# Kernel optimization log

Measured on AMD Instinct MI355X. Metric: run time of the kernel, lower is better.

The kernel has to match this reference:

```python
import jax, jax.numpy as jnp
import numpy as np
from jax import lax

N_QUBITS = 4
N_QLAYERS = 2
C64 = jnp.complex64
PAIRS = [(i, j) for i in range(N_QUBITS) for j in range(i + 1, N_QUBITS)]  # 6 entangling pairs
CNOT = jnp.array([[1, 0, 0, 0], [0, 1, 0, 0], [0, 0, 0, 1], [0, 0, 1, 0]], dtype=C64)


def _rx(t):
    c = jnp.cos(t / 2).astype(C64)
    s = (-1j * jnp.sin(t / 2)).astype(C64)
    return jnp.stack([jnp.stack([c, s]), jnp.stack([s, c])])


def _ry(t):
    c = jnp.cos(t / 2).astype(C64)
    s = jnp.sin(t / 2).astype(C64)
    return jnp.stack([jnp.stack([c, -s]), jnp.stack([s, c])])


def _rz(t):
    e = jnp.exp(-1j * t.astype(C64) / 2)
    z = jnp.zeros_like(e)
    return jnp.stack([jnp.stack([e, z]), jnp.stack([z, jnp.conj(e)])])


def _apply_1q(state, M, w):
    # state: (B,2,2,2,2); M: (2,2) shared or (B,2,2) per-sample
    s = jnp.moveaxis(state, 1 + w, -1)
    if M.ndim == 2:
        s = jnp.einsum('b...j,ij->b...i', s, M)
    else:
        s = jnp.einsum('b...j,bij->b...i', s, M)
    return jnp.moveaxis(s, -1, 1 + w)


def _apply_2q(state, M4, c, t):
    # M4: (4,4) acting on (wire c, wire t)
    s = jnp.moveaxis(state, (1 + c, 1 + t), (-2, -1))
    sh = s.shape
    s = s.reshape(sh[:-2] + (4,))
    s = jnp.einsum('b...j,ij->b...i', s, M4)
    s = s.reshape(sh)
    return jnp.moveaxis(s, (-2, -1), (1 + c, 1 + t))


def _quantum_batched(angles, q_params):
    # angles: (B, 4) classical outputs; encoding is RY(angles*pi)
    B = angles.shape[0]
    state = jnp.zeros((B, 16), C64).at[:, 0].set(1.0).reshape(B, 2, 2, 2, 2)
    theta = angles * jnp.float32(np.pi)
    c = jnp.cos(theta / 2).astype(C64)  # (B,4)
    s = jnp.sin(theta / 2).astype(C64)
    for w in range(N_QUBITS):
        M = jnp.stack([jnp.stack([c[:, w], -s[:, w]], -1),
                       jnp.stack([s[:, w], c[:, w]], -1)], -2)  # (B,2,2)
        state = _apply_1q(state, M, w)
    per_layer = 3 * N_QUBITS + len(PAIRS)  # 18
    for l in range(N_QLAYERS):
        start = l * per_layer
        rot = q_params[start:start + 3 * N_QUBITS].reshape(N_QUBITS, 3)
        ent = q_params[start + 3 * N_QUBITS:start + per_layer]
        for q in range(N_QUBITS):
            M = _rz(rot[q, 2]) @ _ry(rot[q, 1]) @ _rx(rot[q, 0])
            state = _apply_1q(state, M, q)
        for k, (i, j) in enumerate(PAIRS):
            M4 = jnp.kron(jnp.eye(2, dtype=C64), _rz(ent[k])) @ CNOT  # CNOT then RZ on target
            state = _apply_2q(state, M4, i, j)
    probs = jnp.abs(state) ** 2  # (B,2,2,2,2)
    signs = jnp.array([1.0, -1.0], jnp.float32)
    zs = []
    for w in range(N_QUBITS):
        pw = jnp.moveaxis(probs, 1 + w, -1).reshape(B, -1, 2)
        zs.append((pw.sum(1) * signs).sum(-1))
    return jnp.stack(zs, -1)  # (B,4) PauliZ expvals


def _conv(x, w, b):
    y = lax.conv_general_dilated(x, w, (1, 1), ((1, 1), (1, 1)),
                                 dimension_numbers=('NCHW', 'OIHW', 'NCHW'))
    return y + b[None, :, None, None]


def _pool(x):
    return lax.reduce_window(x, -jnp.inf, lax.max, (1, 1, 2, 2), (1, 1, 2, 2), 'VALID')


def setup_inputs() -> dict:
    key = jax.random.key(0)
    ks = jax.random.split(key, 10)
    B = 4096
    return {
        'x': jax.random.normal(ks[0], (B, 1, 28, 28), jnp.float32),
        'conv1_w': jax.random.normal(ks[1], (16, 1, 3, 3), jnp.float32) * 0.1,
        'conv1_b': jax.random.normal(ks[2], (16,), jnp.float32) * 0.1,
        'conv2_w': jax.random.normal(ks[3], (32, 16, 3, 3), jnp.float32) * 0.05,
        'conv2_b': jax.random.normal(ks[4], (32,), jnp.float32) * 0.1,
        'dense_w': jax.random.normal(ks[5], (4, 1568), jnp.float32) * 0.02,
        'dense_b': jax.random.normal(ks[6], (4,), jnp.float32) * 0.1,
        'q_params': jax.random.normal(ks[7], (36,), jnp.float32) * 0.1,
        'post_w': jax.random.normal(ks[8], (10, 4), jnp.float32) * 0.5,
        'post_b': jax.random.normal(ks[9], (10,), jnp.float32) * 0.1,
    }


def reference(x, conv1_w, conv1_b, conv2_w, conv2_b, dense_w, dense_b, q_params, post_w, post_b):
    h = jax.nn.relu(_conv(x, conv1_w, conv1_b))
    h = _pool(h)
    h = jax.nn.relu(_conv(h, conv2_w, conv2_b))
    h = _pool(h)  # (B,32,7,7)
    h = h.reshape(h.shape[0], 32 * 7 * 7)
    # dropout is identity in eval mode
    angles = h @ dense_w.T + dense_b  # (B,4)
    z = _quantum_batched(angles, q_params)  # (B,4)
    return z @ post_w.T + post_b  # (B,10)
```

## Files before the change

kernel.cpp:

```cpp
#include <hip/hip_runtime.h>

#define PI_F 3.14159265358979323846f

typedef _Float16 half2v __attribute__((ext_vector_type(2)));
typedef _Float16 half4v __attribute__((ext_vector_type(4)));
typedef _Float16 half8v __attribute__((ext_vector_type(8)));
typedef float f32x4 __attribute__((ext_vector_type(4)));

struct C2 { float x, y; };
__device__ __forceinline__ C2 cmul(C2 a, C2 b) {
    return C2{a.x * b.x - a.y * b.y, a.x * b.y + a.y * b.x};
}

__device__ __forceinline__ void gate1(float& re, float& im, int l, int w,
                                      C2 m00, C2 m01, C2 m10, C2 m11) {
    int mask = 1 << (3 - w);
    float pre = __shfl_xor(re, mask, 64);
    float pim = __shfl_xor(im, mask, 64);
    bool b = (l & mask) != 0;
    C2 d = b ? m11 : m00;
    C2 o = b ? m10 : m01;
    float nre = d.x * re - d.y * im + o.x * pre - o.y * pim;
    float nim = d.x * im + d.y * re + o.x * pim + o.y * pre;
    re = nre; im = nim;
}

#define WS_C1B 2560
#define WS_DWT 2688
#define WS_GROT 8960
#define WS_GENT 9024

__global__ __launch_bounds__(256) void qnn_prep(
    const float* __restrict__ w1g, const float* __restrict__ w2g,
    const float* __restrict__ dwg, const float* __restrict__ qpg,
    float* __restrict__ ws)
{
    int t = threadIdx.x;
    for (int e = t; e < 640; e += 256) {
        int kstep = e >> 7, rem = e & 127;
        int ntile = rem >> 6, lane = rem & 63;
        int kq = lane >> 4, n = lane & 15;
        int oc = ntile * 16 + n;
        int pi = kstep * 2 + (kq >> 1);
        half8v h;
        #pragma unroll
        for (int jj = 0; jj < 8; ++jj) {
            int ic = (kq & 1) * 8 + jj;
            float v = (pi < 9) ? w2g[oc * 144 + ic * 9 + pi] : 0.f;
            h[jj] = (_Float16)v;
        }
        *(float4*)(ws + e * 4) = __builtin_bit_cast(float4, h);
    }
    if (t < 64) {
        int ky = t >> 4, n = t & 15;
        half4v h;
        #pragma unroll
        for (int j = 0; j < 4; ++j) {
            float v = (ky < 3 && j < 3) ? w1g[n * 9 + ky * 3 + j] : 0.f;
            h[j] = (_Float16)v;
        }
        *(float2*)(ws + WS_C1B + t * 2) = __builtin_bit_cast(float2, h);
    }
    for (int e = t; e < 1568; e += 256) {
        int quad = e >> 5, oc = e & 31;
        int src = oc * 49 + quad;
        float4 v = {dwg[src], dwg[1568 + src], dwg[3136 + src], dwg[4704 + src]};
        *(float4*)(ws + WS_DWT + e * 4) = v;
    }
    if (t < 8) {
        int layer = t >> 2, q = t & 3;
        int st = layer * 18;
        float a0 = qpg[st + 3 * q], a1 = qpg[st + 3 * q + 1], a2 = qpg[st + 3 * q + 2];
        float cx = cosf(0.5f * a0), sx = sinf(0.5f * a0);
        float cy = cosf(0.5f * a1), sy = sinf(0.5f * a1);
        float cz = cosf(0.5f * a2), sz = sinf(0.5f * a2);
        C2 T00{cy * cx,  sy * sx}, T01{-sy * cx, -cy * sx};
        C2 T10{sy * cx, -cy * sx}, T11{ cy * cx, -sy * sx};
        C2 E0{cz, -sz}, E1{cz, sz};
        C2 m00 = cmul(E0, T00), m01 = cmul(E0, T01);
        C2 m10 = cmul(E1, T10), m11 = cmul(E1, T11);
        float* gm = ws + WS_GROT + t * 8;
        gm[0] = m00.x; gm[1] = m00.y; gm[2] = m01.x; gm[3] = m01.y;
        gm[4] = m10.x; gm[5] = m10.y; gm[6] = m11.x; gm[7] = m11.y;
    }
    if (t >= 32 && t < 44) {
        int k = t - 32;
        float e = qpg[(k / 6) * 18 + 12 + (k % 6)];
        ws[WS_GENT + k * 2]     = cosf(0.5f * e);
        ws[WS_GENT + k * 2 + 1] = sinf(0.5f * e);
    }
}

__global__ __launch_bounds__(256, 4) void qnn_fused(
    const float* __restrict__ xg,
    const float* __restrict__ b1g, const float* __restrict__ b2g,
    const float* __restrict__ dbg,
    const float* __restrict__ wsc,
    const float* __restrict__ pwg, const float* __restrict__ pbg,
    float* __restrict__ out, int Btot)
{
    const int b4 = blockIdx.x << 2;
    const int t = threadIdx.x;
    const int lane = t & 63;
    const int wv = __builtin_amdgcn_readfirstlane(t >> 6);
    const int kq = lane >> 4;
    const int lm = lane & 15;

    __shared__ __align__(16) unsigned xhl[1200];
    __shared__ __align__(16) _Float16 p1f[16 * 20 * 24];
    __shared__ __align__(16) float angp[64];

    half8v bC2[5][2];
    {
        const float4* wsB = (const float4*)wsc;
        #pragma unroll
        for (int ks = 0; ks < 5; ++ks)
            #pragma unroll
            for (int nt = 0; nt < 2; ++nt)
                bC2[ks][nt] = __builtin_bit_cast(half8v, wsB[(ks * 2 + nt) * 64 + lane]);
    }
    half4v bC1 = __builtin_bit_cast(half4v, *(const float2*)(wsc + WS_C1B + lane * 2));
    float bias1 = b1g[lm];
    float b20 = b2g[lm], b21 = b2g[16 + lm];

    {
        uint4 z4 = {0u, 0u, 0u, 0u};
        uint4* p4 = (uint4*)p1f;
        #pragma unroll
        for (int j = 0; j < 4; ++j) {
            int i = t + j * 256;
            if (i < 960) p4[i] = z4;
        }
    }

    for (int e = 0; e < 4; ++e) {
        const int bi = b4 + e;
        {
            const float* xb = xg + (size_t)bi * 784;
            int y = t / 40;
            int x = t - y * 40;
            #pragma unroll
            for (int it = 0; it < 5; ++it) {
                int j = t + it * 256;
                if (j < 1200) {
                    float v = 0.f;
                    if (bi < Btot && y >= 1 && y <= 28 && x >= 1 && x <= 28)
                        v = xb[y * 28 + x - 29];
                    _Float16 h = (_Float16)v;
                    _Float16 lo = (_Float16)(v - (float)h);
                    half2v p; p.x = h; p.y = lo;
                    xhl[j] = __builtin_bit_cast(unsigned, p);
                }
                x += 16; y += 6; if (x >= 40) { x -= 40; y += 1; }
            }
        }
        __syncthreads();

        {
            int kyc = (kq < 3) ? kq : 0;
            int pos = lm & 3;
            int pyo = pos >> 1, pxo = pos & 1;
            int p14 = wv * 4 + (lm >> 2);
            int Y = p14 / 14, X = p14 - Y * 14;
            int q14 = wv * 4 + kq;
            int r = q14 / 14, c = q14 - r * 14;
            for (int tile = wv; tile < 49; tile += 4) {
                int py = 2 * Y + pyo, px = 2 * X + pxo;
                int base = (py + kyc) * 40 + px;
                unsigned u0 = xhl[base], u1 = xhl[base + 1], u2 = xhl[base + 2];
                half2v h0 = __builtin_bit_cast(half2v, u0);
                half2v h1 = __builtin_bit_cast(half2v, u1);
                half2v h2 = __builtin_bit_cast(half2v, u2);
                half4v ah = {h0.x, h1.x, h2.x, (_Float16)0.f};
                half4v al = {h0.y, h1.y, h2.y, (_Float16)0.f};
                f32x4 acc = {bias1, bias1, bias1, bias1};
                acc = __builtin_amdgcn_mfma_f32_16x16x16f16(ah, bC1, acc, 0, 0, 0);
                acc = __builtin_amdgcn_mfma_f32_16x16x16f16(al, bC1, acc, 0, 0, 0);
                float v = fmaxf(fmaxf(fmaxf(acc.x, acc.y), fmaxf(acc.z, acc.w)), 0.f);
                p1f[((r + 1) * 20 + (c + 1)) * 24 + lm] = (_Float16)v;
                X += 2; Y += 1; if (X >= 14) { X -= 14; Y += 1; }
                c += 2; r += 1; if (c >= 14) { c -= 14; r += 1; }
            }
        }
        __syncthreads();

        {
            float dp0 = 0.f, dp1 = 0.f, dp2 = 0.f, dp3 = 0.f;
            const float4* dt = (const float4*)(wsc + WS_DWT);
            for (int tile = wv; tile < 13; tile += 4) {
                int m = tile * 16 + lm;
                int quad = m >> 2; if (quad > 48) quad = 48;
                int pos = m & 3;
                int Y = quad / 7, X = quad - Y * 7;
                int py = 2 * Y + (pos >> 1), px = 2 * X + (pos & 1);
                int base0 = py * 20 + px;
                f32x4 acc0 = {b20, b20, b20, b20};
                f32x4 acc1 = {b21, b21, b21, b21};
                int ich = (kq & 1) * 8;
                #pragma unroll
                for (int ks = 0; ks < 5; ++ks) {
                    int pi = ks * 2 + (kq >> 1);
                    if (pi > 8) pi = 8;
                    int ky = (pi >= 6) ? 2 : ((pi >= 3) ? 1 : 0);
                    int kx = pi - ky * 3;
                    half8v a = *(const half8v*)(&p1f[(base0 + ky * 20 + kx) * 24 + ich]);
                    acc0 = __builtin_amdgcn_mfma_f32_16x16x32_f16(a, bC2[ks][0], acc0, 0, 0, 0);
                    acc1 = __builtin_amdgcn_mfma_f32_16x16x32_f16(a, bC2[ks][1], acc1, 0, 0, 0);
                }
                int quadO = tile * 4 + kq;
                if (quadO < 49) {
                    float v0 = fmaxf(fmaxf(fmaxf(acc0.x, acc0.y), fmaxf(acc0.z, acc0.w)), 0.f);
                    float v1 = fmaxf(fmaxf(fmaxf(acc1.x, acc1.y), fmaxf(acc1.z, acc1.w)), 0.f);
                    float4 q0 = dt[quadO * 32 + lm];
                    float4 q1 = dt[quadO * 32 + 16 + lm];
                    dp0 = fmaf(v0, q0.x, fmaf(v1, q1.x, dp0));
                    dp1 = fmaf(v0, q0.y, fmaf(v1, q1.y, dp1));
                    dp2 = fmaf(v0, q0.z, fmaf(v1, q1.z, dp2));
                    dp3 = fmaf(v0, q0.w, fmaf(v1, q1.w, dp3));
                }
            }
            #pragma unroll
            for (int m = 32; m >= 1; m >>= 1) {
                dp0 += __shfl_xor(dp0, m, 64);
                dp1 += __shfl_xor(dp1, m, 64);
                dp2 += __shfl_xor(dp2, m, 64);
                dp3 += __shfl_xor(dp3, m, 64);
            }
            if (lane == 0) {
                float4 dpv = {dp0, dp1, dp2, dp3};
                *(float4*)&angp[e * 16 + wv * 4] = dpv;
            }
        }
        __syncthreads();
    }

    {
        const int bi = b4 + wv;
        const float* ap = angp + wv * 16;
        float4 a0v = *(const float4*)(ap);
        float4 a1v = *(const float4*)(ap + 4);
        float4 a2v = *(const float4*)(ap + 8);
        float4 a3v = *(const float4*)(ap + 12);
        float aw[4] = {a0v.x + a1v.x + a2v.x + a3v.x + dbg[0],
                       a0v.y + a1v.y + a2v.y + a3v.y + dbg[1],
                       a0v.z + a1v.z + a2v.z + a3v.z + dbg[2],
                       a0v.w + a1v.w + a2v.w + a3v.w + dbg[3]};
        int l = lm;
        float re = (l == 0) ? 1.f : 0.f;
        float im = 0.f;
        #pragma unroll
        for (int w = 0; w < 4; ++w) {
            float th = aw[w] * (PI_F * 0.5f);
            float cth = cosf(th), sth = sinf(th);
            gate1(re, im, l, w, C2{cth, 0.f}, C2{-sth, 0.f}, C2{sth, 0.f}, C2{cth, 0.f});
        }
        #pragma unroll
        for (int layer = 0; layer < 2; ++layer) {
            #pragma unroll
            for (int q = 0; q < 4; ++q) {
                const float* gm = wsc + WS_GROT + (layer * 4 + q) * 8;
                gate1(re, im, l, q, C2{gm[0], gm[1]}, C2{gm[2], gm[3]},
                                     C2{gm[4], gm[5]}, C2{gm[6], gm[7]});
            }
            const int pi_[6] = {0, 0, 0, 1, 1, 2};
            const int pj_[6] = {1, 2, 3, 2, 3, 3};
            #pragma unroll
            for (int k = 0; k < 6; ++k) {
                int i = pi_[k], j = pj_[k];
                const float* em = wsc + WS_GENT + (layer * 6 + k) * 2;
                float ce = em[0], se = em[1];
                int maskj = 1 << (3 - j);
                float pre = __shfl_xor(re, maskj, 64);
                float pim = __shfl_xor(im, maskj, 64);
                bool ci = ((l >> (3 - i)) & 1) != 0;
                re = ci ? pre : re;
                im = ci ? pim : im;
                bool bj = (l & maskj) != 0;
                C2 ph{ce, bj ? se : -se};
                C2 rr = cmul(C2{re, im}, ph);
                re = rr.x; im = rr.y;
            }
        }
        float pr = re * re + im * im;
        float z0 = ((l >> 3) & 1) ? -pr : pr;
        float z1 = ((l >> 2) & 1) ? -pr : pr;
        float z2 = ((l >> 1) & 1) ? -pr : pr;
        float z3 = (l & 1)        ? -pr : pr;
        #pragma unroll
        for (int m = 1; m <= 8; m <<= 1) {
            z0 += __shfl_xor(z0, m, 64);
            z1 += __shfl_xor(z1, m, 64);
            z2 += __shfl_xor(z2, m, 64);
            z3 += __shfl_xor(z3, m, 64);
        }
        if (lane < 10 && bi < Btot) {
            float4 pw4 = *(const float4*)(pwg + lane * 4);
            float o = pbg[lane];
            o = fmaf(z0, pw4.x, o); o = fmaf(z1, pw4.y, o);
            o = fmaf(z2, pw4.z, o); o = fmaf(z3, pw4.w, o);
            out[(size_t)bi * 10 + lane] = o;
        }
    }
}

extern "C" void kernel_launch(void* const* d_in, const int* in_sizes, int n_in,
                              void* d_out, int out_size, void* d_ws, size_t ws_size,
                              hipStream_t stream) {
    const float* x  = (const float*)d_in[0];
    const float* w1 = (const float*)d_in[1];
    const float* b1 = (const float*)d_in[2];
    const float* w2 = (const float*)d_in[3];
    const float* b2 = (const float*)d_in[4];
    const float* dw = (const float*)d_in[5];
    const float* db = (const float*)d_in[6];
    const float* qp = (const float*)d_in[7];
    const float* pw = (const float*)d_in[8];
    const float* pb = (const float*)d_in[9];
    float* out = (float*)d_out;
    float* ws  = (float*)d_ws;
    int B = in_sizes[0] / 784;
    int nb = (B + 3) >> 2;

    qnn_prep<<<1, 256, 0, stream>>>(w1, w2, dw, qp, ws);
    qnn_fused<<<nb, 256, 0, stream>>>(x, b1, b2, db, ws, pw, pb, out, B);
}
```

Before: 117.9 us.

## Fold weight prep into one kernel, prefetch next input, stage pooled features in LDS

The separate single-block prep kernel is removed. Every block now packs conv weights, the dense weights and the quantum gate matrices itself, straight from the raw inputs, and the gate matrices go into shared memory. The next sample's image is prefetched into registers while the current one is processed, which removes one barrier per sample. Pooled conv2 outputs are written to LDS and dotted against dense weights held in registers, replacing scattered global float4 reads. The cost is redundant weight loads in every block, about 28 extra registers for the dense weights, and about 6 KB more LDS, which may reduce occupancy.

```diff
diff --git a/kernel.cpp b/kernel.cpp
--- a/kernel.cpp
+++ b/kernel.cpp
@@ -25,48 +25,85 @@
     re = nre; im = nim;
 }
 
-#define WS_C1B 2560
-#define WS_DWT 2688
-#define WS_GROT 8960
-#define WS_GENT 9024
-
-__global__ __launch_bounds__(256) void qnn_prep(
-    const float* __restrict__ w1g, const float* __restrict__ w2g,
-    const float* __restrict__ dwg, const float* __restrict__ qpg,
-    float* __restrict__ ws)
+__global__ __launch_bounds__(256, 4) void qnn_one(
+    const float* __restrict__ xg,
+    const float* __restrict__ w1g, const float* __restrict__ b1g,
+    const float* __restrict__ w2g, const float* __restrict__ b2g,
+    const float* __restrict__ dwg, const float* __restrict__ dbg,
+    const float* __restrict__ qpg,
+    const float* __restrict__ pwg, const float* __restrict__ pbg,
+    float* __restrict__ out, int Btot)
 {
-    int t = threadIdx.x;
-    for (int e = t; e < 640; e += 256) {
-        int kstep = e >> 7, rem = e & 127;
-        int ntile = rem >> 6, lane = rem & 63;
-        int kq = lane >> 4, n = lane & 15;
-        int oc = ntile * 16 + n;
-        int pi = kstep * 2 + (kq >> 1);
-        half8v h;
-        #pragma unroll
-        for (int jj = 0; jj < 8; ++jj) {
-            int ic = (kq & 1) * 8 + jj;
-            float v = (pi < 9) ? w2g[oc * 144 + ic * 9 + pi] : 0.f;
-            h[jj] = (_Float16)v;
-        }
-        *(float4*)(ws + e * 4) = __builtin_bit_cast(float4, h);
-    }
-    if (t < 64) {
-        int ky = t >> 4, n = t & 15;
-        half4v h;
-        #pragma unroll
-        for (int j = 0; j < 4; ++j) {
-            float v = (ky < 3 && j < 3) ? w1g[n * 9 + ky * 3 + j] : 0.f;
-            h[j] = (_Float16)v;
-        }
-        *(float2*)(ws + WS_C1B + t * 2) = __builtin_bit_cast(float2, h);
-    }
-    for (int e = t; e < 1568; e += 256) {
-        int quad = e >> 5, oc = e & 31;
-        int src = oc * 49 + quad;
-        float4 v = {dwg[src], dwg[1568 + src], dwg[3136 + src], dwg[4704 + src]};
-        *(float4*)(ws + WS_DWT + e * 4) = v;
-    }
+    const int b4 = blockIdx.x << 2;
+    const int t = threadIdx.x;
+    const int lane = t & 63;
+    const int wv = __builtin_amdgcn_readfirstlane(t >> 6);
+    const int kq = lane >> 4;
+    const int lm = lane & 15;
+
+    __shared__ __align__(16) unsigned xhl[1200];
+    __shared__ __align__(16) _Float16 p1f[16 * 20 * 24];
+    __shared__ __align__(16) float p2s[1568];
+    __shared__ __align__(16) float angp[64];
+    __shared__ float grot[64];
+    __shared__ float gent[24];
+
+    int xoff[5];
+    {
+        int y = t / 40, x = t - y * 40;
+        #pragma unroll
+        for (int it = 0; it < 5; ++it) {
+            bool ok = (t + it * 256 < 1200) && y >= 1 && y <= 28 && x >= 1 && x <= 28;
+            xoff[it] = ok ? (y * 28 + x - 29) : -1;
+            x += 16; y += 6; if (x >= 40) { x -= 40; y += 1; }
+        }
+    }
+
+    float xr[5];
+    {
+        const float* xb = xg + (size_t)b4 * 784;
+        #pragma unroll
+        for (int it = 0; it < 5; ++it)
+            xr[it] = (xoff[it] >= 0 && b4 < Btot) ? xb[xoff[it]] : 0.f;
+    }
+
+    float dwr0[7], dwr1[7], dwr2[7], dwr3[7];
+    #pragma unroll
+    for (int k2 = 0; k2 < 7; ++k2) {
+        int i = t + k2 * 256;
+        bool ok = i < 1568;
+        dwr0[k2] = ok ? dwg[i] : 0.f;
+        dwr1[k2] = ok ? dwg[1568 + i] : 0.f;
+        dwr2[k2] = ok ? dwg[3136 + i] : 0.f;
+        dwr3[k2] = ok ? dwg[4704 + i] : 0.f;
+    }
+
+    half8v bC2[5][2];
+    #pragma unroll
+    for (int ks = 0; ks < 5; ++ks) {
+        int pi = ks * 2 + (kq >> 1);
+        bool ok = pi < 9;
+        const float* wp0 = w2g + lm * 144 + (kq & 1) * 72 + (ok ? pi : 0);
+        #pragma unroll
+        for (int nt = 0; nt < 2; ++nt) {
+            const float* wp = wp0 + nt * (16 * 144);
+            half8v h;
+            #pragma unroll
+            for (int jj = 0; jj < 8; ++jj)
+                h[jj] = ok ? (_Float16)wp[jj * 9] : (_Float16)0.f;
+            bC2[ks][nt] = h;
+        }
+    }
+
+    half4v bC1 = {(_Float16)0.f, (_Float16)0.f, (_Float16)0.f, (_Float16)0.f};
+    if (kq < 3) {
+        #pragma unroll
+        for (int j = 0; j < 3; ++j)
+            bC1[j] = (_Float16)w1g[lm * 9 + kq * 3 + j];
+    }
+    float bias1 = b1g[lm];
+    float b20 = b2g[lm], b21 = b2g[16 + lm];
+
     if (t < 8) {
         int layer = t >> 2, q = t & 3;
         int st = layer * 18;
@@ -79,49 +116,16 @@
         C2 E0{cz, -sz}, E1{cz, sz};
         C2 m00 = cmul(E0, T00), m01 = cmul(E0, T01);
         C2 m10 = cmul(E1, T10), m11 = cmul(E1, T11);
-        float* gm = ws + WS_GROT + t * 8;
+        float* gm = grot + t * 8;
         gm[0] = m00.x; gm[1] = m00.y; gm[2] = m01.x; gm[3] = m01.y;
         gm[4] = m10.x; gm[5] = m10.y; gm[6] = m11.x; gm[7] = m11.y;
     }
     if (t >= 32 && t < 44) {
         int k = t - 32;
         float e = qpg[(k / 6) * 18 + 12 + (k % 6)];
-        ws[WS_GENT + k * 2]     = cosf(0.5f * e);
-        ws[WS_GENT + k * 2 + 1] = sinf(0.5f * e);
-    }
-}
-
-__global__ __launch_bounds__(256, 4) void qnn_fused(
-    const float* __restrict__ xg,
-    const float* __restrict__ b1g, const float* __restrict__ b2g,
-    const float* __restrict__ dbg,
-    const float* __restrict__ wsc,
-    const float* __restrict__ pwg, const float* __restrict__ pbg,
-    float* __restrict__ out, int Btot)
-{
-    const int b4 = blockIdx.x << 2;
-    const int t = threadIdx.x;
-    const int lane = t & 63;
-    const int wv = __builtin_amdgcn_readfirstlane(t >> 6);
-    const int kq = lane >> 4;
-    const int lm = lane & 15;
-
-    __shared__ __align__(16) unsigned xhl[1200];
-    __shared__ __align__(16) _Float16 p1f[16 * 20 * 24];
-    __shared__ __align__(16) float angp[64];
-
-    half8v bC2[5][2];
-    {
-        const float4* wsB = (const float4*)wsc;
-        #pragma unroll
-        for (int ks = 0; ks < 5; ++ks)
-            #pragma unroll
-            for (int nt = 0; nt < 2; ++nt)
-                bC2[ks][nt] = __builtin_bit_cast(half8v, wsB[(ks * 2 + nt) * 64 + lane]);
-    }
-    half4v bC1 = __builtin_bit_cast(half4v, *(const float2*)(wsc + WS_C1B + lane * 2));
-    float bias1 = b1g[lm];
-    float b20 = b2g[lm], b21 = b2g[16 + lm];
+        gent[k * 2]     = cosf(0.5f * e);
+        gent[k * 2 + 1] = sinf(0.5f * e);
+    }
 
     {
         uint4 z4 = {0u, 0u, 0u, 0u};
@@ -133,29 +137,26 @@
         }
     }
 
+    #pragma unroll
+    for (int it = 0; it < 5; ++it) {
+        int j = t + it * 256;
+        if (it < 4 || j < 1200) {
+            float v = xr[it];
+            _Float16 h = (_Float16)v;
+            _Float16 lo = (_Float16)(v - (float)h);
+            half2v p; p.x = h; p.y = lo;
+            xhl[j] = __builtin_bit_cast(unsigned, p);
+        }
+    }
+    {
+        const float* xb = xg + (size_t)(b4 + 1) * 784;
+        #pragma unroll
+        for (int it = 0; it < 5; ++it)
+            xr[it] = (xoff[it] >= 0 && b4 + 1 < Btot) ? xb[xoff[it]] : 0.f;
+    }
+    __syncthreads();
+
     for (int e = 0; e < 4; ++e) {
-        const int bi = b4 + e;
-        {
-            const float* xb = xg + (size_t)bi * 784;
-            int y = t / 40;
-            int x = t - y * 40;
-            #pragma unroll
-            for (int it = 0; it < 5; ++it) {
-                int j = t + it * 256;
-                if (j < 1200) {
-                    float v = 0.f;
-                    if (bi < Btot && y >= 1 && y <= 28 && x >= 1 && x <= 28)
-                        v = xb[y * 28 + x - 29];
-                    _Float16 h = (_Float16)v;
-                    _Float16 lo = (_Float16)(v - (float)h);
-                    half2v p; p.x = h; p.y = lo;
-                    xhl[j] = __builtin_bit_cast(unsigned, p);
-                }
-                x += 16; y += 6; if (x >= 40) { x -= 40; y += 1; }
-            }
-        }
-        __syncthreads();
-
         {
             int kyc = (kq < 3) ? kq : 0;
             int pos = lm & 3;
@@ -184,9 +185,27 @@
         }
         __syncthreads();
 
+        if (e < 3) {
+            #pragma unroll
+            for (int it = 0; it < 5; ++it) {
+                int j = t + it * 256;
+                if (it < 4 || j < 1200) {
+                    float v = xr[it];
+                    _Float16 h = (_Float16)v;
+                    _Float16 lo = (_Float16)(v - (float)h);
+                    half2v p; p.x = h; p.y = lo;
+                    xhl[j] = __builtin_bit_cast(unsigned, p);
+                }
+            }
+            if (e < 2) {
+                const float* xb = xg + (size_t)(b4 + e + 2) * 784;
+                #pragma unroll
+                for (int it = 0; it < 5; ++it)
+                    xr[it] = (xoff[it] >= 0 && b4 + e + 2 < Btot) ? xb[xoff[it]] : 0.f;
+            }
+        }
+
         {
-            float dp0 = 0.f, dp1 = 0.f, dp2 = 0.f, dp3 = 0.f;
-            const float4* dt = (const float4*)(wsc + WS_DWT);
             for (int tile = wv; tile < 13; tile += 4) {
                 int m = tile * 16 + lm;
                 int quad = m >> 2; if (quad > 48) quad = 48;
@@ -211,12 +230,24 @@
                 if (quadO < 49) {
                     float v0 = fmaxf(fmaxf(fmaxf(acc0.x, acc0.y), fmaxf(acc0.z, acc0.w)), 0.f);
                     float v1 = fmaxf(fmaxf(fmaxf(acc1.x, acc1.y), fmaxf(acc1.z, acc1.w)), 0.f);
-                    float4 q0 = dt[quadO * 32 + lm];
-                    float4 q1 = dt[quadO * 32 + 16 + lm];
-                    dp0 = fmaf(v0, q0.x, fmaf(v1, q1.x, dp0));
-                    dp1 = fmaf(v0, q0.y, fmaf(v1, q1.y, dp1));
-                    dp2 = fmaf(v0, q0.z, fmaf(v1, q1.z, dp2));
-                    dp3 = fmaf(v0, q0.w, fmaf(v1, q1.w, dp3));
+                    p2s[lm * 49 + quadO] = v0;
+                    p2s[784 + lm * 49 + quadO] = v1;
+                }
+            }
+        }
+        __syncthreads();
+
+        {
+            float dp0 = 0.f, dp1 = 0.f, dp2 = 0.f, dp3 = 0.f;
+            #pragma unroll
+            for (int k2 = 0; k2 < 7; ++k2) {
+                int i = t + k2 * 256;
+                if (k2 < 6 || i < 1568) {
+                    float v = p2s[i];
+                    dp0 = fmaf(v, dwr0[k2], dp0);
+                    dp1 = fmaf(v, dwr1[k2], dp1);
+                    dp2 = fmaf(v, dwr2[k2], dp2);
+                    dp3 = fmaf(v, dwr3[k2], dp3);
                 }
             }
             #pragma unroll
@@ -231,8 +262,8 @@
                 *(float4*)&angp[e * 16 + wv * 4] = dpv;
             }
         }
-        __syncthreads();
-    }
+    }
+    __syncthreads();
 
     {
         const int bi = b4 + wv;
@@ -258,7 +289,7 @@
         for (int layer = 0; layer < 2; ++layer) {
             #pragma unroll
             for (int q = 0; q < 4; ++q) {
-                const float* gm = wsc + WS_GROT + (layer * 4 + q) * 8;
+                const float* gm = grot + (layer * 4 + q) * 8;
                 gate1(re, im, l, q, C2{gm[0], gm[1]}, C2{gm[2], gm[3]},
                                      C2{gm[4], gm[5]}, C2{gm[6], gm[7]});
             }
@@ -267,7 +298,7 @@
             #pragma unroll
             for (int k = 0; k < 6; ++k) {
                 int i = pi_[k], j = pj_[k];
-                const float* em = wsc + WS_GENT + (layer * 6 + k) * 2;
+                const float* em = gent + (layer * 6 + k) * 2;
                 float ce = em[0], se = em[1];
                 int maskj = 1 << (3 - j);
                 float pre = __shfl_xor(re, maskj, 64);
@@ -317,10 +348,8 @@
     const float* pw = (const float*)d_in[8];
     const float* pb = (const float*)d_in[9];
     float* out = (float*)d_out;
-    float* ws  = (float*)d_ws;
     int B = in_sizes[0] / 784;
     int nb = (B + 3) >> 2;
 
-    qnn_prep<<<1, 256, 0, stream>>>(w1, w2, dw, qp, ws);
-    qnn_fused<<<nb, 256, 0, stream>>>(x, b1, b2, db, ws, pw, pb, out, B);
+    qnn_one<<<nb, 256, 0, stream>>>(x, w1, b1, w2, b2, dw, db, qp, pw, pb, out, B);
 }
```

After: 149.8 us. +27.1%, slower.
